# Kernel optimization log

Hardware: AMD Instinct MI355X
Metric: run time of the kernel (lower is better)

The kernel has to match this reference:

```python
import jax, jax.numpy as jnp
import numpy as np

B, V, S = 128, 64, 40
D, H, VOC = 256, 256, 20000


def setup_inputs() -> dict:
    key = jax.random.key(0)
    ks = jax.random.split(key, 26)
    g = lambda k, shp: (jax.random.normal(k, shp, dtype=jnp.float32) * 0.02)
    inp = {}
    inp['input_seqs'] = jax.random.randint(ks[0], (B, V, S), 0, VOC + 1)
    inp['mask'] = jnp.zeros((B, V), jnp.float32)
    inp['length'] = jax.random.randint(ks[1], (B,), 1, V + 1)
    inp['seq_time_step'] = jax.random.uniform(ks[2], (B, V), dtype=jnp.float32)
    inp['codemask'] = jnp.zeros((B, V, S), jnp.float32)
    inp['label'] = jax.random.randint(ks[3], (B,), 0, 2)
    # embedding table; padding_idx=-1 in torch == row VOC zeroed
    inp['emb'] = g(ks[4], (VOC + 1, D)).at[VOC].set(0.0)
    # LSTM (single layer, batch_first): torch gate order i,f,g,o
    inp['W_ih'] = g(ks[5], (4 * H, D))
    inp['W_hh'] = g(ks[6], (4 * H, H))
    inp['b_ih'] = g(ks[7], (4 * H,))
    inp['b_hh'] = g(ks[8], (4 * H,))
    # attention projections
    inp['Whk'] = g(ks[9], (D, H))
    inp['bhk'] = g(ks[10], (D,))
    inp['W1'] = g(ks[11], (64, 2 * H))
    inp['b1'] = g(ks[12], (64,))
    inp['W2'] = g(ks[13], (2, 64))
    inp['b2'] = g(ks[14], (2,))
    # classifyer MLP: d -> 4d -> 2d -> 2
    inp['C1W'] = g(ks[15], (4 * D, D))
    inp['C1b'] = g(ks[16], (4 * D,))
    inp['C2W'] = g(ks[17], (2 * D, 4 * D))
    inp['C2b'] = g(ks[18], (2 * D,))
    inp['CoW'] = g(ks[19], (2, 2 * D))
    inp['Cob'] = g(ks[20], (2,))
    return inp


def _lstm(x, W_ih, W_hh, b_ih, b_hh):
    # x: [B,T,D] -> hs: [B,T,H]; torch gate order i,f,g,o
    Bsz = x.shape[0]
    Hd = W_hh.shape[1]
    xg = jnp.einsum('btd,gd->btg', x, W_ih) + b_ih + b_hh  # [B,T,4H]

    def step(carry, xg_t):
        h, c = carry
        gates = xg_t + h @ W_hh.T
        i, f, gg, o = jnp.split(gates, 4, axis=-1)
        i = jax.nn.sigmoid(i); f = jax.nn.sigmoid(f)
        gg = jnp.tanh(gg); o = jax.nn.sigmoid(o)
        c = f * c + i * gg
        h = o * jnp.tanh(c)
        return (h, c), h

    z = jnp.zeros((Bsz, Hd), x.dtype)
    _, hs = jax.lax.scan(step, (z, z), jnp.swapaxes(xg, 0, 1))
    return jnp.swapaxes(hs, 0, 1)


def _classify(h, C1W, C1b, C2W, C2b, CoW, Cob):
    h = jax.nn.relu(h @ C1W.T + C1b)
    h = jax.nn.relu(h @ C2W.T + C2b)
    return h @ CoW.T + Cob


def reference(input_seqs, mask, length, seq_time_step, codemask, label,
              emb, W_ih, W_hh, b_ih, b_hh, Whk, bhk, W1, b1, W2, b2,
              C1W, C1b, C2W, C2b, CoW, Cob):
    # before(): embedding gather -> relu -> sum over codes (eval mode, no dropout)
    v = jax.nn.relu(emb[input_seqs]).sum(-2)  # [B,V,D]
    h = _lstm(v, W_ih, W_hh, b_ih, b_hh)       # [B,V,H]

    # vectorized form of the per-timestep attention loop:
    # bar_v[:,0]=v[:,0]; for i>=1: mix of e_k=v[:,0] and w_hk(h[:,i-1])
    e_k = v[:, :1, :]                                   # [B,1,D]
    wh = h @ Whk.T + bhk                                # [B,V,D]
    wh_prev = wh[:, :-1, :]                             # [B,V-1,D] (h at i-1)
    e_b = jnp.broadcast_to(e_k, wh_prev.shape)
    cat = jnp.concatenate([e_b, wh_prev], axis=-1)      # [B,V-1,2D]
    attn = jax.nn.softmax(jnp.tanh(cat @ W1.T + b1) @ W2.T + b2, axis=-1)
    bar_rest = e_b * attn[..., 0:1] + wh_prev * attn[..., 1:2]
    bar_v = jnp.concatenate([v[:, :1, :], bar_rest], axis=1)  # [B,V,D]

    # GAN stand-in (external injected module): identity
    Dec_V, Gen_V = bar_v, bar_v
    gen_h = _lstm(Gen_V, W_ih, W_hh, b_ih, b_hh)

    og = _classify(h, C1W, C1b, C2W, C2b, CoW, Cob)        # [B,V,2]
    fake = _classify(gen_h, C1W, C1b, C2W, C2b, CoW, Cob)  # [B,V,2]
    final_og = og[:, -1, :]
    final_fake = fake[:, -1, :]
    return (final_og, final_fake, Dec_V, Gen_V, seq_time_step, label)
```

## Files before the change

### kernel.cpp

```cpp
#include <hip/hip_runtime.h>

#define DEV __device__ __forceinline__

typedef float f32x4 __attribute__((ext_vector_type(4)));
typedef short s16x8 __attribute__((ext_vector_type(8)));
typedef short s16x4 __attribute__((ext_vector_type(4)));

DEV unsigned short f2bf(float f){
  unsigned int u = __float_as_uint(f);
  u += 0x7fffu + ((u>>16)&1u);
  return (unsigned short)(u>>16);
}
DEV float bf2f(unsigned short h){ return __uint_as_float(((unsigned int)h)<<16); }

#if __has_builtin(__builtin_amdgcn_rcpf)
DEV float frcp_(float x){ return __builtin_amdgcn_rcpf(x); }
#else
DEV float frcp_(float x){ return 1.f/x; }
#endif
#if __has_builtin(__builtin_amdgcn_exp2f)
DEV float fexp2_(float x){ return __builtin_amdgcn_exp2f(x); }
#else
DEV float fexp2_(float x){ return exp2f(x); }
#endif

DEV float tanh_(float x){
  x = fminf(x, 30.f);
  float e = fexp2_(2.8853900817779268f*x);
  return (e-1.f)*frcp_(e+1.f);
}

DEV unsigned char f2e4m3(float x){
  unsigned int u = __float_as_uint(x);
  unsigned int s = (u>>24)&0x80u;
  unsigned int mag = u & 0x7fffffffu;
  if (mag > 0x43E00000u) mag = 0x43E00000u;
  mag += 0x000FFFFFu + ((mag>>20)&1u);
  int e = (int)(mag>>23) - 120;
  unsigned int m = (mag>>20)&7u;
  unsigned int r = (e<=0) ? 0u : (((unsigned)e<<3)|m);
  return (unsigned char)(s|r);
}

DEV f32x4 mfma_bf16(s16x8 a, s16x8 b, f32x4 c){
  return __builtin_amdgcn_mfma_f32_16x16x32_bf16(a,b,c,0,0,0);
}
DEV f32x4 mfma_fp8(long a, long b, f32x4 c){
  return __builtin_amdgcn_mfma_f32_16x16x32_fp8_fp8(a,b,c,0,0,0);
}

DEV void lds_barrier(){
  asm volatile("s_waitcnt lgkmcnt(0)\n\ts_barrier" ::: "memory");
}

DEV unsigned aload_rlx(unsigned* p){
  return __hip_atomic_load(p, __ATOMIC_RELAXED, __HIP_MEMORY_SCOPE_AGENT);
}
DEV void astore_rlx(unsigned* p, unsigned v){
  __hip_atomic_store(p, v, __ATOMIC_RELAXED, __HIP_MEMORY_SCOPE_AGENT);
}
DEV void aadd_rlx(unsigned* p, unsigned v){
  __hip_atomic_fetch_add(p, v, __ATOMIC_RELAXED, __HIP_MEMORY_SCOPE_AGENT);
}
DEV void acq_fence(){ __builtin_amdgcn_fence(__ATOMIC_ACQUIRE, "agent"); }
DEV void spin_rlx(unsigned* p, unsigned tgt){
  while (aload_rlx(p) < tgt) __builtin_amdgcn_s_sleep(2);
  asm volatile("" ::: "memory");
}
DEV void block_wait(unsigned* p, unsigned tgt){
  if (threadIdx.x == 0) spin_rlx(p, tgt);
  __syncthreads();
}
DEV void block_wait_acq(unsigned* p, unsigned tgt){
  if (threadIdx.x == 0){ spin_rlx(p, tgt); acq_fence(); }
  __syncthreads();
}
DEV s16x4 aload64(const unsigned short* p){
  unsigned long long v = __hip_atomic_load((unsigned long long*)(void*)p,
      __ATOMIC_RELAXED, __HIP_MEMORY_SCOPE_AGENT);
  union { unsigned long long u; s16x4 s; } c; c.u = v; return c.s;
}
DEV void astore64(unsigned short* p, s16x4 v){
  union { s16x4 s; unsigned long long u; } c; c.s = v;
  __hip_atomic_store((unsigned long long*)(void*)p, c.u,
      __ATOMIC_RELAXED, __HIP_MEMORY_SCOPE_AGENT);
}
DEV void astoref(float* p, float v){
  __hip_atomic_store(p, v, __ATOMIC_RELAXED, __HIP_MEMORY_SCOPE_AGENT);
}
DEV void astore16(unsigned short* p, unsigned short v){
  __hip_atomic_store(p, v, __ATOMIC_RELAXED, __HIP_MEMORY_SCOPE_AGENT);
}
DEV void vm_drain(){ asm volatile("s_waitcnt vmcnt(0)" ::: "memory"); }
DEV void ntf(float* p, float v){ __builtin_nontemporal_store(v, p); }

#define Bx 128
#define Vx 64
#define Sx 40
#define Dx 256
#define Hx 256
#define NVOC 20001

#define OFF_OG   0
#define OFF_FAKE 256
#define OFF_DECV 512
#define OFF_GENV 2097664
#define OFF_STS  4194816
#define OFF_LBL  4203008

#define PW_IH  0
#define PW_HH  262144
#define PW_HK  524288
#define PW_1   589824
#define PC_1   622592
#define PC_2   884736
#define PC_O   1409024
#define P_TOT  1410048

#define HPB 264
#define BFP 272
#define WHP 272

#define FCT(t)  ((t)*32)
#define FXG(t)  (2048 + (t)*32)
#define FUC     4096
#define XDONE   4224
#define Y1D     4352
#define Y2D     4480
#define FTOT    8192

__global__ void k_cvt_emb(const float* __restrict__ emb, unsigned short* __restrict__ emb16){
  size_t i = (size_t)blockIdx.x*256 + threadIdx.x;
  emb16[i] = f2bf(emb[i]);
}

__global__ void k_pre(const int* __restrict__ seqs, const unsigned short* __restrict__ emb16,
                      unsigned short* __restrict__ v16,
                      float* __restrict__ decv, float* __restrict__ genv,
                      const float* __restrict__ W_ih, const float* __restrict__ Whh,
                      const float* __restrict__ Whk, const float* __restrict__ W1,
                      const float* __restrict__ C1W, const float* __restrict__ C2W,
                      const float* __restrict__ CoW,
                      unsigned short* __restrict__ pool, unsigned char* __restrict__ whh8,
                      const float* __restrict__ sts, const int* __restrict__ label,
                      float* __restrict__ out, unsigned* __restrict__ flags){
  int bx = blockIdx.x, tid = threadIdx.x;
  if (bx < 8192){
    int bt = bx, d = tid;
    const int* sp = seqs + (size_t)bt*Sx;
    float acc = 0.f;
    #pragma unroll 8
    for (int s=0;s<Sx;s++) acc += fmaxf(bf2f(emb16[(size_t)sp[s]*Dx + d]), 0.f);
    size_t o = (size_t)bt*Dx + d;
    v16[o] = f2bf(acc);
    if ((bt & 63) == 0){ decv[o] = acc; genv[o] = acc; }
    return;
  }
  if (bx < 14724){
    int i = (bx-8192)*256 + tid;
    if (i < P_TOT){
      float v;
      if      (i < PW_HH) v = W_ih[i - PW_IH];
      else if (i < PW_HK) v = Whh [i - PW_HH];
      else if (i < PW_1 ) v = Whk [i - PW_HK];
      else if (i < PC_1 ) v = W1  [i - PW_1 ];
      else if (i < PC_2 ) v = C1W [i - PC_1 ];
      else if (i < PC_O ) v = C2W [i - PC_2 ];
      else                v = CoW [i - PC_O ];
      pool[i] = f2bf(v);
    } else if (i < P_TOT + 262144){
      whh8[i - P_TOT] = f2e4m3(16.f*Whh[i - P_TOT]);
    }
    return;
  }
  for (int i=tid;i<FTOT;i+=256) flags[i] = 0u;
  for (int i=tid;i<Bx*Vx;i+=256) out[OFF_STS + i] = sts[i];
  if (tid < Bx) out[OFF_LBL + tid] = (float)label[tid];
}

template<int MODE_A, int MODE_C, int RELU>
__global__ void k_gemm(const unsigned short* __restrict__ A, const unsigned short* __restrict__ Bw,
                       const float* __restrict__ bias1, const float* __restrict__ bias2,
                       unsigned short* __restrict__ C, int K, int Ntot, float scale){
  int tid = threadIdx.x, w = tid>>6, l = tid&63, lm = l&15, q = l>>4;
  int m0 = blockIdx.x*64;
  int n0 = blockIdx.y*256 + w*64;
  f32x4 acc[4][4];
  #pragma unroll
  for (int nt=0;nt<4;nt++){
    int n = n0 + nt*16 + lm;
    float bz = bias1 ? bias1[n] : 0.f;
    if (bias2) bz += bias2[n];
    #pragma unroll
    for (int mt=0;mt<4;mt++) acc[mt][nt] = (f32x4){bz,bz,bz,bz};
  }
  const s16x8* Arow[4];
  #pragma unroll
  for (int mt=0;mt<4;mt++){
    int m = m0 + mt*16 + lm;
    size_t off = (MODE_A==0) ? (size_t)m*K : ((size_t)(m&127)*Vx + (m>>7))*(size_t)K;
    Arow[mt] = (const s16x8*)(A + off);
  }
  int kkn = K/32;
  for (int kk=0; kk<kkn; kk++){
    s16x8 bfr[4];
    #pragma unroll
    for (int nt=0;nt<4;nt++){
      int n = n0 + nt*16 + lm;
      bfr[nt] = *(const s16x8*)(Bw + (size_t)n*K + kk*32 + q*8);
    }
    #pragma unroll
    for (int mt=0;mt<4;mt++){
      s16x8 afr = Arow[mt][kk*4 + q];
      #pragma unroll
      for (int nt=0;nt<4;nt++)
        acc[mt][nt] = mfma_bf16(afr, bfr[nt], acc[mt][nt]);
    }
  }
  #pragma unroll
  for (int mt=0;mt<4;mt++){
    int mbase = m0 + mt*16 + q*4;
    #pragma unroll
    for (int nt=0;nt<4;nt++){
      int n = n0 + nt*16 + lm;
      if (MODE_C==0){
        #pragma unroll
        for (int r=0;r<4;r++){
          float val = scale*acc[mt][nt][r];
          if (RELU) val = fmaxf(val, 0.f);
          C[(size_t)(mbase+r)*Ntot + n] = f2bf(val);
        }
      } else {
        int tt = mbase>>7, bb = mbase&127;
        int gg = bb>>4;
        s16x4 sv;
        #pragma unroll
        for (int r=0;r<4;r++) sv[r] = (short)f2bf(scale*acc[mt][nt][r]);
        *(s16x4*)(C + (((size_t)tt*8 + gg)*1024 + n)*16 + (bb&15)) = sv;
      }
    }
  }
}

DEV void lstm_act(const f32x4* A, float* cst, float* hv){
  const float K1 = 1.4426950408889634f/256.f;
  #pragma unroll
  for (int r=0;r<4;r++){
    float iv = frcp_(1.f + fexp2_(-K1*A[0][r]));
    float fv = frcp_(1.f + fexp2_(-K1*A[1][r]));
    float eg = fexp2_(2.f*K1*A[2][r]);
    float gv = (eg-1.f)*frcp_(eg+1.f);
    float ov = frcp_(1.f + fexp2_(-K1*A[3][r]));
    float cv = fv*cst[r] + iv*gv;
    cst[r] = cv;
    float ec = fexp2_(2.8853900817779268f*fminf(cv,30.f));
    hv[r] = ov*(ec-1.f)*frcp_(ec+1.f);
  }
}

DEV void store_h_fp8(unsigned char* hn, int q, const float* hv){
#if __has_builtin(__builtin_amdgcn_cvt_pk_fp8_f32)
  int p01 = __builtin_amdgcn_cvt_pk_fp8_f32(16.f*hv[0], 16.f*hv[1], 0, false);
  int p23 = __builtin_amdgcn_cvt_pk_fp8_f32(16.f*hv[2], 16.f*hv[3], 0, false);
  hn[(q*4+0)*HPB] = (unsigned char)p01;
  hn[(q*4+1)*HPB] = (unsigned char)(p01>>8);
  hn[(q*4+2)*HPB] = (unsigned char)p23;
  hn[(q*4+3)*HPB] = (unsigned char)(p23>>8);
#else
  #pragma unroll
  for (int r=0;r<4;r++) hn[(q*4+r)*HPB] = f2e4m3(16.f*hv[r]);
#endif
}

DEV void scan1_body(unsigned char* smem, const unsigned char* __restrict__ W8,
                    const unsigned short* __restrict__ xg1, unsigned short* __restrict__ hist,
                    int g, unsigned* __restrict__ flags){
  unsigned char*  hl  = smem;
  unsigned short* h1b = (unsigned short*)(smem + 8448);
  int tid = threadIdx.x;
  int w = tid>>6, l = tid&63, lm = l&15, q = l>>4;
  int j = w*16 + lm;
  for (int i=tid;i<8448;i+=1024) hl[i] = 0;
  long Bf[4][8];
  #pragma unroll
  for (int qq=0;qq<4;qq++){
    int n = qq*256 + j;
    #pragma unroll
    for (int kk=0;kk<8;kk++)
      Bf[qq][kk] = *(const long*)(W8 + (size_t)n*256 + kk*32 + q*8);
  }
  float cst[4] = {0.f,0.f,0.f,0.f};
  const unsigned short* xgb = xg1 + (size_t)g*16384 + q*4;
  s16x4 xc[4], xn[4];
  #pragma unroll
  for (int qq=0;qq<4;qq++) xc[qq] = *(const s16x4*)(xgb + (qq*256+j)*16);
  __syncthreads();
  const unsigned char* hrd = hl + lm*HPB + q*8;
  #pragma unroll 1
  for (int t=0;t<Vx;t++){
    if (t < Vx-1){
      #pragma unroll
      for (int qq=0;qq<4;qq++)
        xn[qq] = *(const s16x4*)(xgb + (size_t)(t+1)*131072 + (qq*256+j)*16);
    }
    const unsigned char* hb = hrd + (t&1)*4224;
    f32x4 A[4];
    #pragma unroll
    for (int qq=0;qq<4;qq++){
      #pragma unroll
      for (int r=0;r<4;r++) A[qq][r] = bf2f((unsigned short)xc[qq][r]);
    }
    #pragma unroll
    for (int kk=0;kk<8;kk++){
      long af = *(const long*)(hb + kk*32);
      A[0] = mfma_fp8(af, Bf[0][kk], A[0]);
      A[1] = mfma_fp8(af, Bf[1][kk], A[1]);
      A[2] = mfma_fp8(af, Bf[2][kk], A[2]);
      A[3] = mfma_fp8(af, Bf[3][kk], A[3]);
    }
    float hv[4];
    lstm_act(A, cst, hv);
    store_h_fp8(hl + ((t+1)&1)*4224 + j, q, hv);
    #pragma unroll
    for (int r=0;r<4;r++) h1b[(q*4+r)*BFP + j] = f2bf(hv[r]);
    lds_barrier();
    {
      int row = tid>>6, c4 = (tid&63)*4;
      s16x4 hx = *(const s16x4*)(h1b + row*BFP + c4);
      astore64(hist + ((size_t)t*Bx + g*16 + row)*Hx + c4, hx);
    }
    if ((t&3) == 3){
      vm_drain();
      __syncthreads();
      if (tid == 0){
        aadd_rlx(&flags[FCT(t-3)], 1);
        aadd_rlx(&flags[FCT(t-2)], 1);
        aadd_rlx(&flags[FCT(t-1)], 1);
        aadd_rlx(&flags[FCT(t  )], 1);
      }
    } else {
      lds_barrier();
    }
    #pragma unroll
    for (int qq=0;qq<4;qq++) xc[qq] = xn[qq];
  }
  if (tid == 0) aadd_rlx(&flags[XDONE], 1);
}

DEV void scan2_body(unsigned char* smem, const unsigned char* __restrict__ W8,
                    const unsigned short* __restrict__ xg2, unsigned short* __restrict__ h2,
                    int g, unsigned* __restrict__ flags){
  unsigned char*  hl  = smem;
  unsigned short* h1b = (unsigned short*)(smem + 8448);
  int tid = threadIdx.x;
  int w = tid>>6, l = tid&63, lm = l&15, q = l>>4;
  int j = w*16 + lm;
  for (int i=tid;i<8448;i+=1024) hl[i] = 0;
  long Bf[4][8];
  #pragma unroll
  for (int qq=0;qq<4;qq++){
    int n = qq*256 + j;
    #pragma unroll
    for (int kk=0;kk<8;kk++)
      Bf[qq][kk] = *(const long*)(W8 + (size_t)n*256 + kk*32 + q*8);
  }
  float cst[4] = {0.f,0.f,0.f,0.f};
  const unsigned short* xgb = xg2 + (size_t)g*16384 + q*4;
  s16x4 xc[4], xn1[4], xn2[4];
  block_wait(&flags[FXG(0)], 1);
  #pragma unroll
  for (int qq=0;qq<4;qq++) xc[qq] = aload64(xgb + (qq*256+j)*16);
  block_wait(&flags[FXG(1)], 1);
  #pragma unroll
  for (int qq=0;qq<4;qq++) xn1[qq] = aload64(xgb + 131072 + (qq*256+j)*16);
  int skip = 0;
  const unsigned char* hrd = hl + lm*HPB + q*8;
  #pragma unroll 1
  for (int t=0;t<Vx;t++){
    if (t+2 < Vx){
      if (tid == 0){
        if (!skip) spin_rlx(&flags[FXG(t+2)], 1);
        skip = (t+3 < Vx) && (aload_rlx(&flags[FXG(t+3)]) >= 1);
      }
      __syncthreads();
      #pragma unroll
      for (int qq=0;qq<4;qq++)
        xn2[qq] = aload64(xgb + (size_t)(t+2)*131072 + (qq*256+j)*16);
    }
    const unsigned char* hb = hrd + (t&1)*4224;
    f32x4 A[4];
    #pragma unroll
    for (int qq=0;qq<4;qq++){
      #pragma unroll
      for (int r=0;r<4;r++) A[qq][r] = bf2f((unsigned short)xc[qq][r]);
    }
    #pragma unroll
    for (int kk=0;kk<8;kk++){
      long af = *(const long*)(hb + kk*32);
      A[0] = mfma_fp8(af, Bf[0][kk], A[0]);
      A[1] = mfma_fp8(af, Bf[1][kk], A[1]);
      A[2] = mfma_fp8(af, Bf[2][kk], A[2]);
      A[3] = mfma_fp8(af, Bf[3][kk], A[3]);
    }
    float hv[4];
    lstm_act(A, cst, hv);
    store_h_fp8(hl + ((t+1)&1)*4224 + j, q, hv);
    if (t == Vx-1){
      #pragma unroll
      for (int r=0;r<4;r++) h1b[(q*4+r)*BFP + j] = f2bf(hv[r]);
      lds_barrier();
      {
        int row = tid>>6, c4 = (tid&63)*4;
        s16x4 hx = *(const s16x4*)(h1b + row*BFP + c4);
        astore64(h2 + (size_t)(g*16 + row)*Hx + c4, hx);
      }
      vm_drain();
      __syncthreads();
      if (tid == 0) aadd_rlx(&flags[XDONE], 1);
    } else {
      lds_barrier();
    }
    #pragma unroll
    for (int qq=0;qq<4;qq++){ xc[qq] = xn1[qq]; xn1[qq] = xn2[qq]; }
  }
}

template<int ALDS>
DEV void xg2_tile(const unsigned short* Ab, const unsigned short* __restrict__ pool,
                  const float* __restrict__ b_ih, const float* __restrict__ b_hh,
                  unsigned short* __restrict__ xg2, int tile, int w, int lm, int q){
  int mh = (w&1)*64, nb = (w>>1)*128;
  #pragma unroll 1
  for (int sc=0; sc<4; sc++){
    int n0 = nb + sc*32;
    f32x4 acc[4][2];
    #pragma unroll
    for (int nt=0;nt<2;nt++){
      int n = n0 + nt*16 + lm;
      float bz = b_ih[n] + b_hh[n];
      #pragma unroll
      for (int mt=0;mt<4;mt++) acc[mt][nt] = (f32x4){bz,bz,bz,bz};
    }
    #pragma unroll
    for (int kk=0;kk<8;kk++){
      s16x8 bfr[2];
      #pragma unroll
      for (int nt=0;nt<2;nt++){
        int n = n0 + nt*16 + lm;
        bfr[nt] = *(const s16x8*)(pool + PW_IH + (size_t)n*256 + kk*32 + q*8);
      }
      #pragma unroll
      for (int mt=0;mt<4;mt++){
        int row = mh + mt*16 + lm;
        s16x8 afr = ALDS ? *(const s16x8*)(Ab + (size_t)row*WHP + kk*32 + q*8)
                         : *(const s16x8*)(Ab + (size_t)row*Vx*Dx + kk*32 + q*8);
        acc[mt][0] = mfma_bf16(afr, bfr[0], acc[mt][0]);
        acc[mt][1] = mfma_bf16(afr, bfr[1], acc[mt][1]);
      }
    }
    #pragma unroll
    for (int mt=0;mt<4;mt++){
      int m = mh + mt*16 + q*4;
      int gg = m>>4;
      #pragma unroll
      for (int nt=0;nt<2;nt++){
        int n = n0 + nt*16 + lm;
        s16x4 sv;
        #pragma unroll
        for (int r=0;r<4;r++) sv[r] = (short)f2bf(256.f*acc[mt][nt][r]);
        astore64(xg2 + (((size_t)tile*8 + gg)*1024 + n)*16 + (m&15), sv);
      }
    }
  }
}

DEV void worker_body(unsigned short* whs, int t,
    const unsigned short* __restrict__ hist1, const unsigned short* __restrict__ v16,
    const float* __restrict__ u, const unsigned short* __restrict__ pool,
    const float* __restrict__ bhk, const float* __restrict__ W2, const float* __restrict__ b2,
    const float* __restrict__ b_ih, const float* __restrict__ b_hh,
    float* __restrict__ decv, float* __restrict__ genv,
    unsigned short* __restrict__ xg2, unsigned* __restrict__ flags){
  int tid = threadIdx.x, w = tid>>6, l = tid&63, lm = l&15, q = l>>4;
  if (t == 63){
    xg2_tile<0>(v16, pool, b_ih, b_hh, xg2, 0, w, lm, q);
    vm_drain();
    __syncthreads();
    if (tid == 0) astore_rlx(&flags[FXG(0)], 1);
    return;
  }
  block_wait(&flags[FCT(t)], 8);
  {
    int r0 = (w&7)*16, n0 = (w>>3)*128;
    const unsigned short* Ar = hist1 + ((size_t)t*Bx + r0 + lm)*Hx;
    f32x4 acc[8];
    #pragma unroll
    for (int nt=0;nt<8;nt++){
      float bz = bhk[n0 + nt*16 + lm];
      acc[nt] = (f32x4){bz,bz,bz,bz};
    }
    #pragma unroll
    for (int kk=0;kk<8;kk++){
      s16x8 afr = *(const s16x8*)(Ar + kk*32 + q*8);
      #pragma unroll
      for (int nt=0;nt<8;nt++){
        int n = n0 + nt*16 + lm;
        s16x8 bfr = *(const s16x8*)(pool + PW_HK + (size_t)n*256 + kk*32 + q*8);
        acc[nt] = mfma_bf16(afr, bfr, acc[nt]);
      }
    }
    #pragma unroll
    for (int nt=0;nt<8;nt++){
      int n = n0 + nt*16 + lm, mb = r0 + q*4;
      #pragma unroll
      for (int r=0;r<4;r++) whs[(size_t)(mb+r)*WHP + n] = f2bf(acc[nt][r]);
    }
  }
  if (tid == 0) spin_rlx(&flags[FUC], 8);
  __syncthreads();
  if (w < 8){
    int m0l = w*16;
    f32x4 a2[4];
    #pragma unroll
    for (int nt=0;nt<4;nt++){
      int n = nt*16 + lm;
      #pragma unroll
      for (int r=0;r<4;r++) a2[nt][r] = u[(size_t)(m0l + q*4 + r)*64 + n];
    }
    #pragma unroll
    for (int kk=0;kk<8;kk++){
      s16x8 afr = *(const s16x8*)(whs + (size_t)(m0l+lm)*WHP + kk*32 + q*8);
      #pragma unroll
      for (int nt=0;nt<4;nt++){
        int n = nt*16 + lm;
        s16x8 bfr = *(const s16x8*)(pool + PW_1 + (size_t)n*512 + 256 + kk*32 + q*8);
        a2[nt] = mfma_bf16(afr, bfr, a2[nt]);
      }
    }
    float p0a[4] = {0,0,0,0}, p1a[4] = {0,0,0,0};
    #pragma unroll
    for (int nt=0;nt<4;nt++){
      int n = nt*16 + lm;
      float w2a = W2[n], w2b = W2[64+n];
      #pragma unroll
      for (int r=0;r<4;r++){
        float z = tanh_(a2[nt][r]);
        p0a[r] += z*w2a; p1a[r] += z*w2b;
      }
    }
    #pragma unroll
    for (int s=1;s<16;s<<=1){
      #pragma unroll
      for (int r=0;r<4;r++){ p0a[r] += __shfl_xor(p0a[r], s, 16); p1a[r] += __shfl_xor(p1a[r], s, 16); }
    }
    float bb0 = b2[0], bb1 = b2[1];
    int d0 = lm*16;
    #pragma unroll
    for (int r=0;r<4;r++){
      int b = m0l + q*4 + r;
      float g0 = p0a[r]+bb0, g1 = p1a[r]+bb1;
      float al0 = frcp_(1.f + fexp2_(1.4426950408889634f*(g1-g0)));
      float al1 = 1.f - al0;
      const unsigned short* ek = v16 + (size_t)b*Vx*Dx + d0;
      unsigned short* whp = whs + (size_t)b*WHP + d0;
      size_t ob = ((size_t)b*Vx + (t+1))*Dx + d0;
      #pragma unroll
      for (int c=0;c<2;c++){
        s16x8 e8 = *(const s16x8*)(ek + c*8);
        s16x8 w8 = *(const s16x8*)(whp + c*8);
        s16x8 o16;
        #pragma unroll
        for (int jj=0;jj<8;jj++){
          float o = al0*bf2f((unsigned short)e8[jj]) + al1*bf2f((unsigned short)w8[jj]);
          ntf(decv + ob + c*8 + jj, o);
          ntf(genv + ob + c*8 + jj, o);
          o16[jj] = (short)f2bf(o);
        }
        *(s16x8*)(whp + c*8) = o16;
      }
    }
  }
  __syncthreads();
  xg2_tile<1>(whs, pool, b_ih, b_hh, xg2, t+1, w, lm, q);
  vm_drain();
  __syncthreads();
  if (tid == 0) astore_rlx(&flags[FXG(t+1)], 1);
}

DEV void cls_gemm(const unsigned short* __restrict__ A, const unsigned short* __restrict__ Bw,
                  const float* __restrict__ bias, unsigned short* __restrict__ C,
                  int K, int Ntot, int bxx, int byy){
  int tid = threadIdx.x, w = tid>>6, l = tid&63, lm = l&15, q = l>>4;
  int m0 = bxx*64, n0 = byy*256 + w*64;
  f32x4 acc[4][4];
  #pragma unroll
  for (int nt=0;nt<4;nt++){
    int n = n0 + nt*16 + lm;
    float bz = bias[n];
    #pragma unroll
    for (int mt=0;mt<4;mt++) acc[mt][nt] = (f32x4){bz,bz,bz,bz};
  }
  const s16x8* Arow[4];
  #pragma unroll
  for (int mt=0;mt<4;mt++)
    Arow[mt] = (const s16x8*)(A + (size_t)(m0 + mt*16 + lm)*K);
  int kkn = K/32;
  for (int kk=0; kk<kkn; kk++){
    s16x8 bfr[4];
    #pragma unroll
    for (int nt=0;nt<4;nt++){
      int n = n0 + nt*16 + lm;
      bfr[nt] = *(const s16x8*)(Bw + (size_t)n*K + kk*32 + q*8);
    }
    #pragma unroll
    for (int mt=0;mt<4;mt++){
      s16x8 afr = Arow[mt][kk*4 + q];
      #pragma unroll
      for (int nt=0;nt<4;nt++)
        acc[mt][nt] = mfma_bf16(afr, bfr[nt], acc[mt][nt]);
    }
  }
  #pragma unroll
  for (int mt=0;mt<4;mt++){
    int mbase = m0 + mt*16 + q*4;
    #pragma unroll
    for (int nt=0;nt<4;nt++){
      int n = n0 + nt*16 + lm;
      #pragma unroll
      for (int r=0;r<4;r++)
        astore16(C + (size_t)(mbase+r)*Ntot + n, f2bf(fmaxf(acc[mt][nt][r], 0.f)));
    }
  }
}

__global__ __launch_bounds__(1024) void k_mega(
    const unsigned char* __restrict__ W8,
    unsigned short* __restrict__ xg1, unsigned short* __restrict__ xg2,
    unsigned short* __restrict__ hist1,
    const unsigned short* __restrict__ v16, float* __restrict__ u,
    const unsigned short* __restrict__ pool,
    const float* __restrict__ bhk, const float* __restrict__ W2, const float* __restrict__ b2,
    const float* __restrict__ b1, const float* __restrict__ b_ih, const float* __restrict__ b_hh,
    const float* __restrict__ C1b, const float* __restrict__ C2b, const float* __restrict__ Cob,
    float* __restrict__ decv, float* __restrict__ genv, float* __restrict__ out,
    unsigned* __restrict__ flags){
  __shared__ __align__(16) unsigned char smem[69632];
  int blk = blockIdx.x;
  unsigned short* X  = hist1 + (size_t)(Vx-1)*Bx*Hx;
  unsigned short* h2 = hist1 + (size_t)Vx*Bx*Hx;
  unsigned short* y1 = xg1;
  unsigned short* y2 = xg1 + 262144;
  if (blk < 8){
    scan1_body(smem, W8, xg1, hist1, blk, flags);
  } else if (blk < 16){
    scan2_body(smem, W8, xg2, h2, blk-8, flags);
  } else if (blk < 80){
    worker_body((unsigned short*)smem, blk-16, hist1, v16, u, pool, bhk, W2, b2,
                b_ih, b_hh, decv, genv, xg2, flags);
  } else if (blk < 88){
    int t2 = (blk-80)*1024 + threadIdx.x;
    int b = t2>>6, n = t2&63;
    const s16x8* vr = (const s16x8*)(v16 + (size_t)b*Vx*Dx);
    const s16x8* wr = (const s16x8*)(pool + PW_1 + (size_t)n*512);
    float a = b1[n];
    for (int kk=0;kk<32;kk++){
      s16x8 x = vr[kk], ww = wr[kk];
      #pragma unroll
      for (int jj=0;jj<8;jj++) a += bf2f((unsigned short)x[jj])*bf2f((unsigned short)ww[jj]);
    }
    astoref(u + t2, a);
    vm_drain();
    __syncthreads();
    if (threadIdx.x == 0) aadd_rlx(&flags[FUC], 1);
  } else if (blk < 104){
    block_wait_acq(&flags[XDONE], 16);
    int p = blk-88;
    if (threadIdx.x < 256) cls_gemm(X, pool+PC_1, C1b, y1, 256, 1024, p&3, p>>2);
    vm_drain();
    __syncthreads();
    if (threadIdx.x == 0) aadd_rlx(&flags[Y1D], 1);
  } else if (blk < 112){
    block_wait_acq(&flags[Y1D], 16);
    int p = blk-104;
    if (threadIdx.x < 256) cls_gemm(y1, pool+PC_2, C2b, y2, 1024, 512, p&3, p>>2);
    vm_drain();
    __syncthreads();
    if (threadIdx.x == 0) aadd_rlx(&flags[Y2D], 1);
  } else {
    block_wait_acq(&flags[Y2D], 8);
    if (threadIdx.x < 256){
      int t2 = (blk-112)*256 + threadIdx.x;
      int m = t2>>1, n = t2&1;
      const s16x8* yr = (const s16x8*)(y2 + (size_t)m*512);
      const s16x8* wr = (const s16x8*)(pool + PC_O + (size_t)n*512);
      float a = Cob[n];
      for (int kk=0;kk<64;kk++){
        s16x8 yv = yr[kk], ww = wr[kk];
        #pragma unroll
        for (int jj=0;jj<8;jj++) a += bf2f((unsigned short)yv[jj])*bf2f((unsigned short)ww[jj]);
      }
      int base = (m < 128) ? (OFF_OG + m*2) : (OFF_FAKE + (m-128)*2);
      out[base + n] = a;
    }
  }
}

extern "C" void kernel_launch(void* const* d_in, const int* in_sizes, int n_in,
                              void* d_out, int out_size, void* d_ws, size_t ws_size,
                              hipStream_t stream) {
  const int*   seqs  = (const int*)d_in[0];
  const float* sts   = (const float*)d_in[3];
  const int*   label = (const int*)d_in[5];
  const float* emb   = (const float*)d_in[6];
  const float* W_ih  = (const float*)d_in[7];
  const float* W_hh  = (const float*)d_in[8];
  const float* b_ih  = (const float*)d_in[9];
  const float* b_hh  = (const float*)d_in[10];
  const float* Whk   = (const float*)d_in[11];
  const float* bhk   = (const float*)d_in[12];
  const float* W1    = (const float*)d_in[13];
  const float* b1    = (const float*)d_in[14];
  const float* W2    = (const float*)d_in[15];
  const float* b2    = (const float*)d_in[16];
  const float* C1b   = (const float*)d_in[18];
  const float* C2b   = (const float*)d_in[20];
  const float* Cob   = (const float*)d_in[22];
  float* out = (float*)d_out;

  char* ws = (char*)d_ws;
  unsigned short* v16    = (unsigned short*)(ws + 0);
  unsigned short* xg1    = (unsigned short*)(ws + (4<<20));
  unsigned short* hist1  = (unsigned short*)(ws + (20<<20));
  unsigned short* xg2    = (unsigned short*)(ws + (25<<20));
  unsigned short* emb16  = xg2;
  float*          u      = (float*)(ws + (41<<20));
  unsigned char*  whh8   = (unsigned char*)(ws + (41<<20) + (64<<10));
  unsigned*       flags  = (unsigned*)(ws + (41<<20) + (384<<10));
  unsigned short* pool   = (unsigned short*)(ws + (42<<20));

  float* decv = out + OFF_DECV;
  float* genv = out + OFF_GENV;

  k_cvt_emb<<<dim3(NVOC), dim3(256), 0, stream>>>(emb, emb16);
  k_pre<<<dim3(14725), dim3(256), 0, stream>>>(seqs, emb16, v16, decv, genv,
      W_ih, W_hh, Whk, W1, (const float*)d_in[17], (const float*)d_in[19],
      (const float*)d_in[21], pool, whh8, sts, label, out, flags);
  k_gemm<1,1,0><<<dim3(128,4), dim3(256), 0, stream>>>(v16, pool+PW_IH, b_ih, b_hh, xg1, 256, 1024, 256.f);
  k_mega<<<dim3(114), dim3(1024), 0, stream>>>(whh8, xg1, xg2, hist1, v16, u, pool,
      bhk, W2, b2, b1, b_ih, b_hh, C1b, C2b, Cob, decv, genv, out, flags);
}
```

Measured before the change: 498.9 us.

## Drop embedding bf16 pre-conversion, signal scan1 progress every step, use plain xg2 loads

```diff
diff --git a/kernel.cpp b/kernel.cpp
--- a/kernel.cpp
+++ b/kernel.cpp
@@ -75,11 +75,6 @@
   if (threadIdx.x == 0){ spin_rlx(p, tgt); acq_fence(); }
   __syncthreads();
 }
-DEV s16x4 aload64(const unsigned short* p){
-  unsigned long long v = __hip_atomic_load((unsigned long long*)(void*)p,
-      __ATOMIC_RELAXED, __HIP_MEMORY_SCOPE_AGENT);
-  union { unsigned long long u; s16x4 s; } c; c.u = v; return c.s;
-}
 DEV void astore64(unsigned short* p, s16x4 v){
   union { s16x4 s; unsigned long long u; } c; c.s = v;
   __hip_atomic_store((unsigned long long*)(void*)p, c.u,
@@ -129,12 +124,7 @@
 #define Y2D     4480
 #define FTOT    8192
 
-__global__ void k_cvt_emb(const float* __restrict__ emb, unsigned short* __restrict__ emb16){
-  size_t i = (size_t)blockIdx.x*256 + threadIdx.x;
-  emb16[i] = f2bf(emb[i]);
-}
-
-__global__ void k_pre(const int* __restrict__ seqs, const unsigned short* __restrict__ emb16,
+__global__ void k_pre(const int* __restrict__ seqs, const float* __restrict__ emb,
                       unsigned short* __restrict__ v16,
                       float* __restrict__ decv, float* __restrict__ genv,
                       const float* __restrict__ W_ih, const float* __restrict__ Whh,
@@ -150,7 +140,7 @@
     const int* sp = seqs + (size_t)bt*Sx;
     float acc = 0.f;
     #pragma unroll 8
-    for (int s=0;s<Sx;s++) acc += fmaxf(bf2f(emb16[(size_t)sp[s]*Dx + d]), 0.f);
+    for (int s=0;s<Sx;s++) acc += fmaxf(emb[(size_t)sp[s]*Dx + d], 0.f);
     size_t o = (size_t)bt*Dx + d;
     v16[o] = f2bf(acc);
     if ((bt & 63) == 0){ decv[o] = acc; genv[o] = acc; }
@@ -298,6 +288,11 @@
   const unsigned char* hrd = hl + lm*HPB + q*8;
   #pragma unroll 1
   for (int t=0;t<Vx;t++){
+    if (t > 0){
+      vm_drain();
+      __syncthreads();
+      if (tid == 0) aadd_rlx(&flags[FCT(t-1)], 1);
+    }
     if (t < Vx-1){
       #pragma unroll
       for (int qq=0;qq<4;qq++)
@@ -329,22 +324,12 @@
       s16x4 hx = *(const s16x4*)(h1b + row*BFP + c4);
       astore64(hist + ((size_t)t*Bx + g*16 + row)*Hx + c4, hx);
     }
-    if ((t&3) == 3){
-      vm_drain();
-      __syncthreads();
-      if (tid == 0){
-        aadd_rlx(&flags[FCT(t-3)], 1);
-        aadd_rlx(&flags[FCT(t-2)], 1);
-        aadd_rlx(&flags[FCT(t-1)], 1);
-        aadd_rlx(&flags[FCT(t  )], 1);
-      }
-    } else {
-      lds_barrier();
-    }
     #pragma unroll
     for (int qq=0;qq<4;qq++) xc[qq] = xn[qq];
   }
-  if (tid == 0) aadd_rlx(&flags[XDONE], 1);
+  vm_drain();
+  __syncthreads();
+  if (tid == 0){ aadd_rlx(&flags[FCT(63)], 1); aadd_rlx(&flags[XDONE], 1); }
 }
 
 DEV void scan2_body(unsigned char* smem, const unsigned char* __restrict__ W8,
@@ -369,10 +354,10 @@
   s16x4 xc[4], xn1[4], xn2[4];
   block_wait(&flags[FXG(0)], 1);
   #pragma unroll
-  for (int qq=0;qq<4;qq++) xc[qq] = aload64(xgb + (qq*256+j)*16);
+  for (int qq=0;qq<4;qq++) xc[qq] = *(const s16x4*)(xgb + (qq*256+j)*16);
   block_wait(&flags[FXG(1)], 1);
   #pragma unroll
-  for (int qq=0;qq<4;qq++) xn1[qq] = aload64(xgb + 131072 + (qq*256+j)*16);
+  for (int qq=0;qq<4;qq++) xn1[qq] = *(const s16x4*)(xgb + 131072 + (qq*256+j)*16);
   int skip = 0;
   const unsigned char* hrd = hl + lm*HPB + q*8;
   #pragma unroll 1
@@ -385,7 +370,7 @@
       __syncthreads();
       #pragma unroll
       for (int qq=0;qq<4;qq++)
-        xn2[qq] = aload64(xgb + (size_t)(t+2)*131072 + (qq*256+j)*16);
+        xn2[qq] = *(const s16x4*)(xgb + (size_t)(t+2)*131072 + (qq*256+j)*16);
     }
     const unsigned char* hb = hrd + (t&1)*4224;
     f32x4 A[4];
@@ -732,7 +717,6 @@
   unsigned short* xg1    = (unsigned short*)(ws + (4<<20));
   unsigned short* hist1  = (unsigned short*)(ws + (20<<20));
   unsigned short* xg2    = (unsigned short*)(ws + (25<<20));
-  unsigned short* emb16  = xg2;
   float*          u      = (float*)(ws + (41<<20));
   unsigned char*  whh8   = (unsigned char*)(ws + (41<<20) + (64<<10));
   unsigned*       flags  = (unsigned*)(ws + (41<<20) + (384<<10));
@@ -741,8 +725,7 @@
   float* decv = out + OFF_DECV;
   float* genv = out + OFF_GENV;
 
-  k_cvt_emb<<<dim3(NVOC), dim3(256), 0, stream>>>(emb, emb16);
-  k_pre<<<dim3(14725), dim3(256), 0, stream>>>(seqs, emb16, v16, decv, genv,
+  k_pre<<<dim3(14725), dim3(256), 0, stream>>>(seqs, emb, v16, decv, genv,
       W_ih, W_hh, Whk, W1, (const float*)d_in[17], (const float*)d_in[19],
       (const float*)d_in[21], pool, whh8, sts, label, out, flags);
   k_gemm<1,1,0><<<dim3(128,4), dim3(256), 0, stream>>>(v16, pool+PW_IH, b_ih, b_hh, xg1, 256, 1024, 256.f);
```

Result: slower. 514.4 us (+3.1%).
